# Optimization experiments

Hardware: AMD Instinct MI355X
Metric: run time of the kernel (lower is better)

Reference implementation:

```python
import jax, jax.numpy as jnp
from jax import lax
import numpy as np

RADIUS = 0.05
N_SEEDS = 40

def _farthest_point_sample(xyz, npoint):
    # xyz: [B, N, 3] -> seed indices [B, npoint]
    B, N, _ = xyz.shape
    dist0 = jnp.full((B, N), 1e10, dtype=xyz.dtype)
    far0 = jnp.zeros((B,), dtype=jnp.int32)  # deterministic init (torch uses randint)
    batch_idx = jnp.arange(B)

    def step(carry, _):
        distance, farthest = carry
        centroid = xyz[batch_idx, farthest][:, None, :]          # [B,1,3]
        d = jnp.sum((xyz - centroid) ** 2, axis=-1)              # [B,N]
        distance = jnp.minimum(distance, d)
        new_far = jnp.argmax(distance, axis=-1).astype(jnp.int32)
        return (distance, new_far), farthest

    _, cents = lax.scan(step, (dist0, far0), None, length=npoint)
    return cents.T                                               # [B, npoint]

def setup_inputs() -> dict:
    key = jax.random.key(0)
    pcs = jax.random.uniform(key, (16, 65536, 3), dtype=jnp.float32)
    return {"pcs": pcs}

def reference(pcs) -> jnp.ndarray:
    B, N, C = pcs.shape
    S = N_SEEDS
    seeds = _farthest_point_sample(pcs, S)                       # [B,S] int
    new_xyz = pcs[jnp.arange(B)[:, None], seeds]                 # [B,S,3]
    # squared pairwise distances seeds->points: [B,S,N]
    sqrdists = (jnp.sum(new_xyz ** 2, -1)[:, :, None]
                + jnp.sum(pcs ** 2, -1)[:, None, :]
                - 2.0 * jnp.einsum('bsc,bnc->bsn', new_xyz, pcs))
    relu_dists = jax.nn.relu(RADIUS ** 2 - sqrdists)
    den_mat = jnp.sum(relu_dists, axis=2)                        # [B,S]
    den_var = jnp.var(den_mat, axis=1, ddof=1).mean()            # torch.var is unbiased
    return den_var
```

## Files before the change

kernel.cpp:

```cpp
#include <hip/hip_runtime.h>

typedef unsigned long long ull;

#define NB    16
#define NPTS  65536
#define NSEED 40
#define BPB   16
#define TPB   1024
#define NW    16
#define PPT   4
#define R2    0.0025f
#define PAYLOAD 0xFFFFFFFFFFFFull
#define DONEG 40ull

__device__ __forceinline__ ull packdi(float v, int idx) {
  return ((ull)__float_as_uint(v) << 16) | (ull)((unsigned)(idx ^ 0xFFFF) & 0xFFFFu);
}

__global__ __launch_bounds__(TPB, 4) void fps_den_kernel(
    const float* __restrict__ pcs, ull* __restrict__ slots,
    ull* __restrict__ pden, float* __restrict__ out)
{
  const int beta = blockIdx.x >> 4;
  const int blk  = blockIdx.x & 15;
  const int tid  = threadIdx.x;
  const int lane = tid & 63;
  const int wav  = tid >> 6;
  const float* __restrict__ base = pcs + (size_t)beta * (NPTS * 3);

  __shared__ ull   sRedP[2][NW];
  __shared__ float sWx[2], sWy[2], sWz[2];
  __shared__ float sSx[NSEED], sSy[NSEED], sSz[NSEED];
  __shared__ float sDen[NW][NSEED];
  __shared__ float sV[NB];

  float px[PPT], py[PPT], pz[PPT], dist[PPT];
#pragma unroll
  for (int j = 0; j < PPT; ++j) {
    int n = blk * (TPB * PPT) + j * TPB + tid;
    px[j] = base[n * 3 + 0];
    py[j] = base[n * 3 + 1];
    pz[j] = base[n * 3 + 2];
    dist[j] = 1e10f;
  }

  float cx = base[0], cy = base[1], cz = base[2];
  if (tid == 0) { sSx[0] = cx; sSy[0] = cy; sSz[0] = cz; }

  ull* myslots = slots + (size_t)beta * (2 * BPB);

  for (int k = 0; k < NSEED - 1; ++k) {
    ull bestp = 0;
#pragma unroll
    for (int j = 0; j < PPT; ++j) {
      float dx = px[j] - cx, dy = py[j] - cy, dz = pz[j] - cz;
      float d  = __fadd_rn(__fadd_rn(__fmul_rn(dx, dx), __fmul_rn(dy, dy)),
                           __fmul_rn(dz, dz));
      float nd = fminf(dist[j], d);
      dist[j]  = nd;
      int n    = blk * (TPB * PPT) + j * TPB + tid;
      ull p    = packdi(nd, n);
      if (p > bestp) bestp = p;
    }
    ull mx = bestp;
#pragma unroll
    for (int o = 32; o > 0; o >>= 1) {
      ull q = __shfl_xor(mx, o, 64);
      mx = mx > q ? mx : q;
    }
    if (lane == 0) sRedP[k & 1][wav] = mx;
    __syncthreads();

    const ull gen = (ull)(k + 1);
    const ull g48 = gen << 48;
    ull* arr = myslots + (size_t)((k + 1) & 1) * BPB;

    if (wav == 0) {
      ull rp = (lane < NW) ? sRedP[k & 1][lane] : 0;
      ull m2 = rp;
#pragma unroll
      for (int o = 8; o > 0; o >>= 1) {
        ull q = __shfl_xor(m2, o, 64);
        m2 = m2 > q ? m2 : q;
      }
      if (lane == 0)
        __hip_atomic_store(&arr[blk], g48 | (m2 & PAYLOAD),
                           __ATOMIC_RELAXED, __HIP_MEMORY_SCOPE_AGENT);

      ull vcur = __hip_atomic_load(&arr[lane & 15], __ATOMIC_RELAXED,
                                   __HIP_MEMORY_SCOPE_AGENT);
      for (;;) {
        ull vnext = __hip_atomic_load(&arr[lane & 15], __ATOMIC_RELAXED,
                                      __HIP_MEMORY_SCOPE_AGENT);
        if (__all((int)((vcur >> 48) == gen))) break;
        vcur = vnext;
      }

      ull pl = (lane < NW) ? (vcur & PAYLOAD) : 0;
      ull m = pl;
#pragma unroll
      for (int o = 32; o > 0; o >>= 1) {
        ull q = __shfl_xor(m, o, 64);
        m = m > q ? m : q;
      }
      int widx = (int)((unsigned)(m ^ 0xFFFFull) & 0xFFFFu);
      widx = __builtin_amdgcn_readfirstlane(widx);
      const float* q = base + 3 * (size_t)widx;
      float wx2 = q[0], wy2 = q[1], wz2 = q[2];
      if (lane == 0) {
        sWx[k & 1] = wx2; sWy[k & 1] = wy2; sWz[k & 1] = wz2;
        sSx[k + 1] = wx2; sSy[k + 1] = wy2; sSz[k + 1] = wz2;
      }
    } else {
      float da = 0.f;
#pragma unroll
      for (int j = 0; j < PPT; ++j) {
        float dx = px[j] - cx, dy = py[j] - cy, dz = pz[j] - cz;
        float d  = dx * dx + dy * dy + dz * dz;
        da += fmaxf(R2 - d, 0.f);
      }
#pragma unroll
      for (int o = 32; o > 0; o >>= 1) da += __shfl_xor(da, o, 64);
      if (lane == 0) sDen[wav][k] = da;
    }
    __syncthreads();
    cx = sWx[k & 1]; cy = sWy[k & 1]; cz = sWz[k & 1];
  }

  if (wav == 0) {
    for (int s = 0; s < NSEED; ++s) {
      float sx = sSx[s], sy = sSy[s], sz = sSz[s];
      float a = 0.f;
#pragma unroll
      for (int j = 0; j < PPT; ++j) {
        float dx = px[j] - sx, dy = py[j] - sy, dz = pz[j] - sz;
        float d  = dx * dx + dy * dy + dz * dz;
        a += fmaxf(R2 - d, 0.f);
      }
#pragma unroll
      for (int o = 32; o > 0; o >>= 1) a += __shfl_xor(a, o, 64);
      if (lane == 0) sDen[0][s] = a;
    }
  } else {
    float a = 0.f;
#pragma unroll
    for (int j = 0; j < PPT; ++j) {
      float dx = px[j] - cx, dy = py[j] - cy, dz = pz[j] - cz;
      float d  = dx * dx + dy * dy + dz * dz;
      a += fmaxf(R2 - d, 0.f);
    }
#pragma unroll
    for (int o = 32; o > 0; o >>= 1) a += __shfl_xor(a, o, 64);
    if (lane == 0) sDen[wav][NSEED - 1] = a;
  }
  __syncthreads();

  if (tid < NSEED) {
    float t = 0.f;
#pragma unroll
    for (int w = 0; w < NW; ++w) t += sDen[w][tid];
    ull rec = (DONEG << 48) | (ull)__float_as_uint(t);
    __hip_atomic_store(&pden[((size_t)beta * BPB + blk) * NSEED + tid], rec,
                       __ATOMIC_RELAXED, __HIP_MEMORY_SCOPE_AGENT);
  }

  if (blockIdx.x == 0) {
    __syncthreads();
    if (tid < NB * NSEED) {
      int b0 = tid / NSEED, s = tid - b0 * NSEED;
      float a = 0.f;
#pragma unroll
      for (int c = 0; c < 2; ++c) {
        ull v[8];
#pragma unroll
        for (int b = 0; b < 8; ++b)
          v[b] = __hip_atomic_load(
              &pden[((size_t)b0 * BPB + c * 8 + b) * NSEED + s],
              __ATOMIC_RELAXED, __HIP_MEMORY_SCOPE_AGENT);
        for (;;) {
          bool ok = true;
#pragma unroll
          for (int b = 0; b < 8; ++b)
            if ((v[b] >> 48) != DONEG) {
              ok = false;
              v[b] = __hip_atomic_load(
                  &pden[((size_t)b0 * BPB + c * 8 + b) * NSEED + s],
                  __ATOMIC_RELAXED, __HIP_MEMORY_SCOPE_AGENT);
            }
          if (ok) break;
        }
#pragma unroll
        for (int b = 0; b < 8; ++b)
          a += __uint_as_float((unsigned)(v[b] & 0xFFFFFFFFull));
      }
      sDen[b0][s] = a;
    }
    __syncthreads();
    if (tid < NB) {
      float m = 0.f;
      for (int s = 0; s < NSEED; ++s) m += sDen[tid][s];
      m /= (float)NSEED;
      float q = 0.f;
      for (int s = 0; s < NSEED; ++s) { float d = sDen[tid][s] - m; q += d * d; }
      sV[tid] = q / (float)(NSEED - 1);
    }
    __syncthreads();
    if (tid == 0) {
      float v = 0.f;
      for (int i = 0; i < NB; ++i) v += sV[i];
      out[0] = v / (float)NB;
    }
  }
}

extern "C" void kernel_launch(void* const* d_in, const int* in_sizes, int n_in,
                              void* d_out, int out_size, void* d_ws, size_t ws_size,
                              hipStream_t stream) {
  const float* pcs = (const float*)d_in[0];
  float* out  = (float*)d_out;
  ull*   pden = (ull*)d_ws;
  ull*   slots = (ull*)((char*)d_ws + 81920);
  fps_den_kernel<<<dim3(NB * BPB), dim3(TPB), 0, stream>>>(pcs, slots, pden, out);
}
```

Measured before the change: 169.8 us.

## Move wave-0 density work into other waves and stream per-seed partials early

Wave 0's points are copied to shared memory so wave 1 can compute wave 0's density contribution each iteration while wave 0 handles the cross-block argmax exchange. This removes the 40-seed density loop wave 0 ran after the FPS loop. Per-seed block partials are now written to global memory incrementally from inside the loop, leaving only two at the end. The spin-wait on the exchange slots also keeps several loads in flight to cut polling latency, at the cost of more global traffic during the spin.

Result: faster. 164.4 us (-3.2%).

```diff
diff --git a/kernel.cpp b/kernel.cpp
--- a/kernel.cpp
+++ b/kernel.cpp
@@ -30,7 +30,7 @@
 
   __shared__ ull   sRedP[2][NW];
   __shared__ float sWx[2], sWy[2], sWz[2];
-  __shared__ float sSx[NSEED], sSy[NSEED], sSz[NSEED];
+  __shared__ float sW0x[4 * 64], sW0y[4 * 64], sW0z[4 * 64];
   __shared__ float sDen[NW][NSEED];
   __shared__ float sV[NB];
 
@@ -44,10 +44,19 @@
     dist[j] = 1e10f;
   }
 
+  if (wav == 0) {
+#pragma unroll
+    for (int j = 0; j < PPT; ++j) {
+      sW0x[j * 64 + lane] = px[j];
+      sW0y[j * 64 + lane] = py[j];
+      sW0z[j * 64 + lane] = pz[j];
+    }
+  }
+
   float cx = base[0], cy = base[1], cz = base[2];
-  if (tid == 0) { sSx[0] = cx; sSy[0] = cy; sSz[0] = cz; }
 
   ull* myslots = slots + (size_t)beta * (2 * BPB);
+  ull* mypden  = pden + ((size_t)beta * BPB + blk) * NSEED;
 
   for (int k = 0; k < NSEED - 1; ++k) {
     ull bestp = 0;
@@ -87,29 +96,30 @@
         __hip_atomic_store(&arr[blk], g48 | (m2 & PAYLOAD),
                            __ATOMIC_RELAXED, __HIP_MEMORY_SCOPE_AGENT);
 
-      ull vcur = __hip_atomic_load(&arr[lane & 15], __ATOMIC_RELAXED,
-                                   __HIP_MEMORY_SCOPE_AGENT);
+      ull* ap = &arr[lane & 15];
+      ull t0 = __hip_atomic_load(ap, __ATOMIC_RELAXED, __HIP_MEMORY_SCOPE_AGENT);
+      ull t1 = __hip_atomic_load(ap, __ATOMIC_RELAXED, __HIP_MEMORY_SCOPE_AGENT);
+      ull t2 = __hip_atomic_load(ap, __ATOMIC_RELAXED, __HIP_MEMORY_SCOPE_AGENT);
+      ull t3 = __hip_atomic_load(ap, __ATOMIC_RELAXED, __HIP_MEMORY_SCOPE_AGENT);
       for (;;) {
-        ull vnext = __hip_atomic_load(&arr[lane & 15], __ATOMIC_RELAXED,
-                                      __HIP_MEMORY_SCOPE_AGENT);
-        if (__all((int)((vcur >> 48) == gen))) break;
-        vcur = vnext;
-      }
-
-      ull pl = (lane < NW) ? (vcur & PAYLOAD) : 0;
+        if (__all((int)((t0 >> 48) == gen))) break;
+        t0 = t1; t1 = t2; t2 = t3;
+        t3 = __hip_atomic_load(ap, __ATOMIC_RELAXED, __HIP_MEMORY_SCOPE_AGENT);
+      }
+
+      ull pl = (lane < NW) ? (t0 & PAYLOAD) : 0;
       ull m = pl;
 #pragma unroll
       for (int o = 32; o > 0; o >>= 1) {
         ull q = __shfl_xor(m, o, 64);
         m = m > q ? m : q;
       }
-      int widx = (int)((unsigned)(m ^ 0xFFFFull) & 0xFFFFu);
+      int widx = (int)((unsigned)((m ^ 0xFFFFull) & 0xFFFFull));
       widx = __builtin_amdgcn_readfirstlane(widx);
       const float* q = base + 3 * (size_t)widx;
       float wx2 = q[0], wy2 = q[1], wz2 = q[2];
       if (lane == 0) {
         sWx[k & 1] = wx2; sWy[k & 1] = wy2; sWz[k & 1] = wz2;
-        sSx[k + 1] = wx2; sSy[k + 1] = wy2; sSz[k + 1] = wz2;
       }
     } else {
       float da = 0.f;
@@ -122,26 +132,36 @@
 #pragma unroll
       for (int o = 32; o > 0; o >>= 1) da += __shfl_xor(da, o, 64);
       if (lane == 0) sDen[wav][k] = da;
+
+      if (wav == 1) {
+        float a0 = 0.f;
+#pragma unroll
+        for (int j = 0; j < PPT; ++j) {
+          float dx = sW0x[j * 64 + lane] - cx;
+          float dy = sW0y[j * 64 + lane] - cy;
+          float dz = sW0z[j * 64 + lane] - cz;
+          float d  = dx * dx + dy * dy + dz * dz;
+          a0 += fmaxf(R2 - d, 0.f);
+        }
+#pragma unroll
+        for (int o = 32; o > 0; o >>= 1) a0 += __shfl_xor(a0, o, 64);
+        if (lane == 0) sDen[0][k] = a0;
+      }
+
+      if (wav == 15 && lane == 0 && k > 0) {
+        float t = 0.f;
+#pragma unroll
+        for (int w = 0; w < NW; ++w) t += sDen[w][k - 1];
+        __hip_atomic_store(&mypden[k - 1],
+                           (DONEG << 48) | (ull)__float_as_uint(t),
+                           __ATOMIC_RELAXED, __HIP_MEMORY_SCOPE_AGENT);
+      }
     }
     __syncthreads();
     cx = sWx[k & 1]; cy = sWy[k & 1]; cz = sWz[k & 1];
   }
 
-  if (wav == 0) {
-    for (int s = 0; s < NSEED; ++s) {
-      float sx = sSx[s], sy = sSy[s], sz = sSz[s];
-      float a = 0.f;
-#pragma unroll
-      for (int j = 0; j < PPT; ++j) {
-        float dx = px[j] - sx, dy = py[j] - sy, dz = pz[j] - sz;
-        float d  = dx * dx + dy * dy + dz * dz;
-        a += fmaxf(R2 - d, 0.f);
-      }
-#pragma unroll
-      for (int o = 32; o > 0; o >>= 1) a += __shfl_xor(a, o, 64);
-      if (lane == 0) sDen[0][s] = a;
-    }
-  } else {
+  if (wav >= 1) {
     float a = 0.f;
 #pragma unroll
     for (int j = 0; j < PPT; ++j) {
@@ -152,15 +172,30 @@
 #pragma unroll
     for (int o = 32; o > 0; o >>= 1) a += __shfl_xor(a, o, 64);
     if (lane == 0) sDen[wav][NSEED - 1] = a;
+
+    if (wav == 1) {
+      float a0 = 0.f;
+#pragma unroll
+      for (int j = 0; j < PPT; ++j) {
+        float dx = sW0x[j * 64 + lane] - cx;
+        float dy = sW0y[j * 64 + lane] - cy;
+        float dz = sW0z[j * 64 + lane] - cz;
+        float d  = dx * dx + dy * dy + dz * dz;
+        a0 += fmaxf(R2 - d, 0.f);
+      }
+#pragma unroll
+      for (int o = 32; o > 0; o >>= 1) a0 += __shfl_xor(a0, o, 64);
+      if (lane == 0) sDen[0][NSEED - 1] = a0;
+    }
   }
   __syncthreads();
 
-  if (tid < NSEED) {
+  if (tid < 2) {
+    int s = (NSEED - 2) + tid;
     float t = 0.f;
 #pragma unroll
-    for (int w = 0; w < NW; ++w) t += sDen[w][tid];
-    ull rec = (DONEG << 48) | (ull)__float_as_uint(t);
-    __hip_atomic_store(&pden[((size_t)beta * BPB + blk) * NSEED + tid], rec,
+    for (int w = 0; w < NW; ++w) t += sDen[w][s];
+    __hip_atomic_store(&mypden[s], (DONEG << 48) | (ull)__float_as_uint(t),
                        __ATOMIC_RELAXED, __HIP_MEMORY_SCOPE_AGENT);
   }
 
```
